# Performance work log

Hardware: AMD Instinct MI355X
Metric: run time of the kernel (lower is better)

Reference implementation:

```python
import jax, jax.numpy as jnp
import numpy as np

NUM_LEVELS = 8
CODEBOOK_SIZE = 1024
D_MODEL = 512


def setup_inputs() -> dict:
    key = jax.random.key(0)
    kx, kc = jax.random.split(key)
    x = jax.random.normal(kx, (8, 4096, D_MODEL), dtype=jnp.float32)
    # stacked embedding tables, one per RVQ level: [L, K, D]
    codebooks = jax.random.normal(kc, (NUM_LEVELS, CODEBOOK_SIZE, D_MODEL), dtype=jnp.float32)
    return {"x": x, "codebooks": codebooks}


def reference(x, codebooks):
    """Residual VQ: per level, nearest-codebook lookup on the residual.

    x: [B, N, D], codebooks: [L, K, D].
    Returns (quantized [B, N, D] with straight-through estimator, indices [B, N, L]).
    """
    residual = x
    q_sum = jnp.zeros_like(x)
    all_indices = []
    for l in range(codebooks.shape[0]):
        cb = codebooks[l]  # [K, D]
        # squared Euclidean distance; argmin matches torch.cdist argmin
        r2 = jnp.sum(residual * residual, axis=-1, keepdims=True)      # [B, N, 1]
        c2 = jnp.sum(cb * cb, axis=-1)                                  # [K]
        cross = jnp.einsum("bnd,kd->bnk", residual, cb)                # [B, N, K]
        dist2 = r2 - 2.0 * cross + c2                                   # [B, N, K]
        idx = jnp.argmin(dist2, axis=-1)                                # [B, N]
        all_indices.append(idx)
        q = cb[idx]                                                     # gather: [B, N, D]
        q_sum = q_sum + q
        residual = residual - q
    # straight-through: forward value is q_sum, gradient flows to x only
    quantized = x + jax.lax.stop_gradient(q_sum - x)
    return quantized, jnp.stack(all_indices, axis=-1)
```

## Files before the change

kernel.cpp:

```cpp
#include <hip/hip_runtime.h>
#include <stdint.h>

#define NLV 8
#define KCB 1024
#define DM  512
#define NTOK (8*4096)

typedef _Float16 f16;
typedef f16  f16x4 __attribute__((ext_vector_type(4)));
typedef f16  f16x8 __attribute__((ext_vector_type(8)));
typedef float f32x4 __attribute__((ext_vector_type(4)));

#define SPLIT_SCALE 2048.0f
#define INV_SPLIT   (1.0f/2048.0f)

typedef __attribute__((address_space(1))) const unsigned int* as1p;
typedef __attribute__((address_space(3))) unsigned int*       as3p;
__device__ __forceinline__ void gll16(const void* g, void* l) {
    __builtin_amdgcn_global_load_lds((as1p)g, (as3p)l, 16, 0, 0);
}

__global__ void c2_kernel(const float* __restrict__ cbs, float* __restrict__ c2) {
    int row  = blockIdx.x;
    int lane = threadIdx.x;
    const float4* p4 = (const float4*)(cbs + (size_t)row * DM);
    float4 a = p4[lane];
    float4 b = p4[lane + 64];
    float s = a.x*a.x + a.y*a.y + a.z*a.z + a.w*a.w
            + b.x*b.x + b.y*b.y + b.z*b.z + b.w*b.w;
    #pragma unroll
    for (int off = 32; off > 0; off >>= 1) s += __shfl_down(s, off, 64);
    if (lane == 0) c2[row] = s;
}

__global__ void split_kernel(const float* __restrict__ src,
                             f16* __restrict__ hi, f16* __restrict__ lo) {
    size_t i = (size_t)blockIdx.x * 256 + threadIdx.x;
    float4 v = ((const float4*)src)[i];
    f16x4 h, l;
    h.x = (f16)v.x; l.x = (f16)((v.x - (float)h.x) * SPLIT_SCALE);
    h.y = (f16)v.y; l.y = (f16)((v.y - (float)h.y) * SPLIT_SCALE);
    h.z = (f16)v.z; l.z = (f16)((v.z - (float)h.z) * SPLIT_SCALE);
    h.w = (f16)v.w; l.w = (f16)((v.w - (float)h.w) * SPLIT_SCALE);
    ((f16x4*)hi)[i] = h;
    ((f16x4*)lo)[i] = l;
}

#define MB   128
#define NCH  256
#define KS   32
#define NTHR 512
#define BUFB 49152

__global__ __launch_bounds__(NTHR, 2)
void rvq_mfma(const float* __restrict__ xin, float* __restrict__ qout,
              const float* __restrict__ cbs,
              const f16* __restrict__ Bhi, const f16* __restrict__ Blo,
              f16* __restrict__ Ahi, f16* __restrict__ Alo,
              const float* __restrict__ c2g, float* __restrict__ idxout,
              int lvl, int is_last)
{
    __shared__ char smem[2 * BUFB];
    const int tid  = threadIdx.x;
    const int lane = tid & 63;
    const int wid  = tid >> 6;
    const int wm   = wid >> 2;
    const int wn   = wid & 3;
    const int tx   = lane & 15;
    const int q    = lane >> 4;
    const size_t tok0 = (size_t)blockIdx.x * MB;

    const f16*   Bh_l = Bhi + (size_t)lvl * KCB * DM;
    const f16*   Bl_l = Blo + (size_t)lvl * KCB * DM;
    const float* c2l  = c2g + lvl * KCB;
    const float* cbl  = cbs + (size_t)lvl * KCB * DM;

    const int stg  = (tid & 3) ^ ((tid >> 3) & 3);
    const int srow = tid >> 2;
    const int rsw  = q ^ ((tx >> 1) & 3);

    auto stage = [&](char* bb, int cb0, int k0) {
        const int ko = k0 + stg * 8;
        const size_t arow = (tok0 + srow) * (size_t)DM + ko;
        gll16(&Ahi[arow], bb +     0 + wid * 1024);
        gll16(&Alo[arow], bb +  8192 + wid * 1024);
        const size_t br0 = (size_t)(cb0 + srow)       * DM + ko;
        const size_t br1 = (size_t)(cb0 + 128 + srow) * DM + ko;
        gll16(&Bh_l[br0], bb + 16384        + wid * 1024);
        gll16(&Bh_l[br1], bb + 16384 + 8192 + wid * 1024);
        gll16(&Bl_l[br0], bb + 32768        + wid * 1024);
        gll16(&Bl_l[br1], bb + 32768 + 8192 + wid * 1024);
    };

    float bestv[16];
    int   besti[16];
    #pragma unroll
    for (int t = 0; t < 16; ++t) { bestv[t] = 3.4e38f; besti[t] = 0; }

    stage(smem, 0, 0);

    for (int ch = 0; ch < KCB / NCH; ++ch) {
        const int cb0 = ch * NCH;
        f32x4 ahh[4][4], axx[4][4];
        #pragma unroll
        for (int i = 0; i < 4; ++i)
            #pragma unroll
            for (int j = 0; j < 4; ++j) { ahh[i][j] = (f32x4)0.0f; axx[i][j] = (f32x4)0.0f; }

        for (int kk = 0; kk < DM / KS; ++kk) {
            char* bb  = smem + (kk & 1) * BUFB;
            char* bbn = smem + ((kk & 1) ^ 1) * BUFB;
            __syncthreads();
            if (kk < DM / KS - 1)      stage(bbn, cb0, (kk + 1) * KS);
            else if (ch < KCB/NCH - 1) stage(bbn, cb0 + NCH, 0);

            const f16* sAh = (const f16*)(bb);
            const f16* sAl = (const f16*)(bb + 8192);
            const f16* sBh = (const f16*)(bb + 16384);
            const f16* sBl = (const f16*)(bb + 32768);

            f16x8 ah[4], al[4];
            #pragma unroll
            for (int i = 0; i < 4; ++i) {
                int off = (wm * 64 + i * 16 + tx) * 32 + rsw * 8;
                ah[i] = *(const f16x8*)&sAh[off];
                al[i] = *(const f16x8*)&sAl[off];
            }
            #pragma unroll
            for (int j = 0; j < 4; ++j) {
                int boff = (wn * 64 + j * 16 + tx) * 32 + rsw * 8;
                f16x8 bh = *(const f16x8*)&sBh[boff];
                f16x8 bl = *(const f16x8*)&sBl[boff];
                #pragma unroll
                for (int i = 0; i < 4; ++i) {
                    ahh[i][j] = __builtin_amdgcn_mfma_f32_16x16x32_f16(ah[i], bh, ahh[i][j], 0, 0, 0);
                    axx[i][j] = __builtin_amdgcn_mfma_f32_16x16x32_f16(ah[i], bl, axx[i][j], 0, 0, 0);
                    axx[i][j] = __builtin_amdgcn_mfma_f32_16x16x32_f16(al[i], bh, axx[i][j], 0, 0, 0);
                }
            }
        }

        #pragma unroll
        for (int j = 0; j < 4; ++j) {
            int n = cb0 + wn * 64 + j * 16 + tx;
            float c2v = c2l[n];
            #pragma unroll
            for (int i = 0; i < 4; ++i)
                #pragma unroll
                for (int r = 0; r < 4; ++r) {
                    float dot = ahh[i][j][r] + axx[i][j][r] * INV_SPLIT;
                    float s = fmaf(-2.f, dot, c2v);
                    int t = i * 4 + r;
                    if (s < bestv[t]) { bestv[t] = s; besti[t] = n; }
                }
        }
    }

    #pragma unroll
    for (int t = 0; t < 16; ++t) {
        float v = bestv[t]; int bi = besti[t];
        #pragma unroll
        for (int off = 1; off < 16; off <<= 1) {
            float ov = __shfl_xor(v, off, 64);
            int   oi = __shfl_xor(bi, off, 64);
            if (ov < v || (ov == v && oi < bi)) { v = ov; bi = oi; }
        }
        bestv[t] = v; besti[t] = bi;
    }

    float* redV = (float*)smem;
    int*   redI = (int*)(smem + 2048);
    int*   kbst = (int*)(smem + 4096);
    __syncthreads();
    if (tx == 0) {
        #pragma unroll
        for (int i = 0; i < 4; ++i)
            #pragma unroll
            for (int r = 0; r < 4; ++r) {
                int m = i * 16 + q * 4 + r;
                redV[(wm * 4 + wn) * 64 + m] = bestv[i * 4 + r];
                redI[(wm * 4 + wn) * 64 + m] = besti[i * 4 + r];
            }
    }
    __syncthreads();
    if (tid < MB) {
        int mwm = tid >> 6, m = tid & 63;
        float bv = redV[(mwm * 4) * 64 + m];
        int   bi = redI[(mwm * 4) * 64 + m];
        #pragma unroll
        for (int w = 1; w < 4; ++w) {
            float v  = redV[(mwm * 4 + w) * 64 + m];
            int   ii = redI[(mwm * 4 + w) * 64 + m];
            if (v < bv || (v == bv && ii < bi)) { bv = v; bi = ii; }
        }
        kbst[tid] = bi;
        idxout[(tok0 + tid) * NLV + lvl] = (float)bi;
    }
    __syncthreads();

    for (int it = 0; it < 16; ++it) {
        int e  = it * NTHR + tid;
        int t  = e >> 6, d8 = e & 63;
        size_t go = (tok0 + t) * (size_t)DM + d8 * 8;
        f16x8 h8 = *(const f16x8*)&Ahi[go];
        f16x8 l8 = *(const f16x8*)&Alo[go];
        const float* cp = &cbl[(size_t)kbst[t] * DM + d8 * 8];
        float4 c0 = *(const float4*)cp;
        float4 c1 = *(const float4*)(cp + 4);
        float r[8];
        r[0] = (float)h8[0] + (float)l8[0] * INV_SPLIT - c0.x;
        r[1] = (float)h8[1] + (float)l8[1] * INV_SPLIT - c0.y;
        r[2] = (float)h8[2] + (float)l8[2] * INV_SPLIT - c0.z;
        r[3] = (float)h8[3] + (float)l8[3] * INV_SPLIT - c0.w;
        r[4] = (float)h8[4] + (float)l8[4] * INV_SPLIT - c1.x;
        r[5] = (float)h8[5] + (float)l8[5] * INV_SPLIT - c1.y;
        r[6] = (float)h8[6] + (float)l8[6] * INV_SPLIT - c1.z;
        r[7] = (float)h8[7] + (float)l8[7] * INV_SPLIT - c1.w;
        if (is_last) {
            float4 x0 = *(const float4*)&xin[go];
            float4 x1 = *(const float4*)&xin[go + 4];
            float4 q0 = make_float4(x0.x - r[0], x0.y - r[1], x0.z - r[2], x0.w - r[3]);
            float4 q1 = make_float4(x1.x - r[4], x1.y - r[5], x1.z - r[6], x1.w - r[7]);
            *(float4*)&qout[go]     = q0;
            *(float4*)&qout[go + 4] = q1;
        } else {
            f16x8 h, l;
            #pragma unroll
            for (int k = 0; k < 8; ++k) {
                h[k] = (f16)r[k];
                l[k] = (f16)((r[k] - (float)h[k]) * SPLIT_SCALE);
            }
            *(f16x8*)&Ahi[go] = h;
            *(f16x8*)&Alo[go] = l;
        }
    }
}

extern "C" void kernel_launch(void* const* d_in, const int* in_sizes, int n_in,
                              void* d_out, int out_size, void* d_ws, size_t ws_size,
                              hipStream_t stream) {
    const float* x   = (const float*)d_in[0];
    const float* cbs = (const float*)d_in[1];
    float* qout   = (float*)d_out;
    float* idxout = qout + (size_t)NTOK * DM;

    const size_t B_ELE = (size_t)NLV * KCB * DM;
    const size_t A_ELE = (size_t)NTOK * DM;

    f16* Bhi = (f16*)d_ws;
    f16* Blo = Bhi + B_ELE;
    f16* Ahi = Blo + B_ELE;
    f16* Alo = Ahi + A_ELE;
    float* c2 = (float*)(Alo + A_ELE);

    split_kernel<<<(int)(B_ELE / 4 / 256), 256, 0, stream>>>(cbs, Bhi, Blo);
    split_kernel<<<(int)(A_ELE / 4 / 256), 256, 0, stream>>>(x, Ahi, Alo);
    c2_kernel<<<NLV * KCB, 64, 0, stream>>>(cbs, c2);

    const int nblocks = NTOK / MB;
    for (int l = 0; l < NLV; ++l) {
        rvq_mfma<<<nblocks, NTHR, 0, stream>>>(x, qout, cbs,
                                               Bhi, Blo, Ahi, Alo, c2, idxout,
                                               l, (l == NLV - 1) ? 1 : 0);
    }
}
```

Baseline: 1.152 ms.

## Shrink token tile, load A from registers, fold split correction into one accumulator

```diff
diff --git a/kernel.cpp b/kernel.cpp
--- a/kernel.cpp
+++ b/kernel.cpp
@@ -5,14 +5,12 @@
 #define KCB 1024
 #define DM  512
 #define NTOK (8*4096)
+#define BETA 0.00390625f
 
 typedef _Float16 f16;
 typedef f16  f16x4 __attribute__((ext_vector_type(4)));
 typedef f16  f16x8 __attribute__((ext_vector_type(8)));
 typedef float f32x4 __attribute__((ext_vector_type(4)));
-
-#define SPLIT_SCALE 2048.0f
-#define INV_SPLIT   (1.0f/2048.0f)
 
 typedef __attribute__((address_space(1))) const unsigned int* as1p;
 typedef __attribute__((address_space(3))) unsigned int*       as3p;
@@ -28,9 +26,14 @@
     float4 b = p4[lane + 64];
     float s = a.x*a.x + a.y*a.y + a.z*a.z + a.w*a.w
             + b.x*b.x + b.y*b.y + b.z*b.z + b.w*b.w;
-    #pragma unroll
-    for (int off = 32; off > 0; off >>= 1) s += __shfl_down(s, off, 64);
-    if (lane == 0) c2[row] = s;
+    float t = (float)(f16)a.x + (float)(f16)a.y + (float)(f16)a.z + (float)(f16)a.w
+            + (float)(f16)b.x + (float)(f16)b.y + (float)(f16)b.z + (float)(f16)b.w;
+    #pragma unroll
+    for (int off = 32; off > 0; off >>= 1) {
+        s += __shfl_down(s, off, 64);
+        t += __shfl_down(t, off, 64);
+    }
+    if (lane == 0) c2[row] = s + 2.0f * BETA * t;
 }
 
 __global__ void split_kernel(const float* __restrict__ src,
@@ -38,21 +41,20 @@
     size_t i = (size_t)blockIdx.x * 256 + threadIdx.x;
     float4 v = ((const float4*)src)[i];
     f16x4 h, l;
-    h.x = (f16)v.x; l.x = (f16)((v.x - (float)h.x) * SPLIT_SCALE);
-    h.y = (f16)v.y; l.y = (f16)((v.y - (float)h.y) * SPLIT_SCALE);
-    h.z = (f16)v.z; l.z = (f16)((v.z - (float)h.z) * SPLIT_SCALE);
-    h.w = (f16)v.w; l.w = (f16)((v.w - (float)h.w) * SPLIT_SCALE);
+    h.x = (f16)v.x; l.x = (f16)((v.x - (float)h.x) + BETA);
+    h.y = (f16)v.y; l.y = (f16)((v.y - (float)h.y) + BETA);
+    h.z = (f16)v.z; l.z = (f16)((v.z - (float)h.z) + BETA);
+    h.w = (f16)v.w; l.w = (f16)((v.w - (float)h.w) + BETA);
     ((f16x4*)hi)[i] = h;
     ((f16x4*)lo)[i] = l;
 }
 
-#define MB   128
+#define MBT  64
 #define NCH  256
 #define KS   32
 #define NTHR 512
-#define BUFB 49152
-
-__global__ __launch_bounds__(NTHR, 2)
+
+__global__ __launch_bounds__(NTHR, 4)
 void rvq_mfma(const float* __restrict__ xin, float* __restrict__ qout,
               const float* __restrict__ cbs,
               const f16* __restrict__ Bhi, const f16* __restrict__ Blo,
@@ -60,7 +62,7 @@
               const float* __restrict__ c2g, float* __restrict__ idxout,
               int lvl, int is_last)
 {
-    __shared__ char smem[2 * BUFB];
+    __shared__ char smem[65536];
     const int tid  = threadIdx.x;
     const int lane = tid & 63;
     const int wid  = tid >> 6;
@@ -68,75 +70,87 @@
     const int wn   = wid & 3;
     const int tx   = lane & 15;
     const int q    = lane >> 4;
-    const size_t tok0 = (size_t)blockIdx.x * MB;
+    const size_t tok0 = (size_t)blockIdx.x * MBT;
 
     const f16*   Bh_l = Bhi + (size_t)lvl * KCB * DM;
     const f16*   Bl_l = Blo + (size_t)lvl * KCB * DM;
     const float* c2l  = c2g + lvl * KCB;
     const float* cbl  = cbs + (size_t)lvl * KCB * DM;
 
-    const int stg  = (tid & 3) ^ ((tid >> 3) & 3);
     const int srow = tid >> 2;
-    const int rsw  = q ^ ((tx >> 1) & 3);
-
-    auto stage = [&](char* bb, int cb0, int k0) {
-        const int ko = k0 + stg * 8;
-        const size_t arow = (tok0 + srow) * (size_t)DM + ko;
-        gll16(&Ahi[arow], bb +     0 + wid * 1024);
-        gll16(&Alo[arow], bb +  8192 + wid * 1024);
-        const size_t br0 = (size_t)(cb0 + srow)       * DM + ko;
-        const size_t br1 = (size_t)(cb0 + 128 + srow) * DM + ko;
-        gll16(&Bh_l[br0], bb + 16384        + wid * 1024);
-        gll16(&Bh_l[br1], bb + 16384 + 8192 + wid * 1024);
-        gll16(&Bl_l[br0], bb + 32768        + wid * 1024);
-        gll16(&Bl_l[br1], bb + 32768 + 8192 + wid * 1024);
+    const int sg   = (tid & 3) ^ ((srow >> 1) & 3);
+    auto stageB = [&](char* buf, int cb0, int k0) {
+        const int ko = k0 + sg * 8;
+        const size_t g0 = (size_t)(cb0 + srow) * DM + ko;
+        const size_t g1 = g0 + (size_t)128 * DM;
+        char* l0 = buf + wid * 1024;
+        gll16(&Bh_l[g0], l0);
+        gll16(&Bh_l[g1], l0 + 8192);
+        gll16(&Bl_l[g0], l0 + 16384);
+        gll16(&Bl_l[g1], l0 + 16384 + 8192);
     };
 
-    float bestv[16];
-    int   besti[16];
-    #pragma unroll
-    for (int t = 0; t < 16; ++t) { bestv[t] = 3.4e38f; besti[t] = 0; }
-
-    stage(smem, 0, 0);
+    int boff[4];
+    #pragma unroll
+    for (int j = 0; j < 4; ++j) {
+        int row = wn * 64 + j * 16 + tx;
+        boff[j] = row * 64 + (q ^ ((tx >> 1) & 3)) * 16;
+    }
+
+    const f16* aH = Ahi + (tok0 + wm * 32 + tx) * (size_t)DM + q * 8;
+    const f16* aL = Alo + (tok0 + wm * 32 + tx) * (size_t)DM + q * 8;
+
+    float bestv[8];
+    int   besti[8];
+    #pragma unroll
+    for (int t = 0; t < 8; ++t) { bestv[t] = 3.4e38f; besti[t] = 0; }
+
+    f16x8 Ah[2][2], Al[2][2];
+    #pragma unroll
+    for (int i = 0; i < 2; ++i) {
+        Ah[0][i] = *(const f16x8*)(aH + i * 16 * DM);
+        Al[0][i] = *(const f16x8*)(aL + i * 16 * DM);
+    }
+    stageB(smem, 0, 0);
 
     for (int ch = 0; ch < KCB / NCH; ++ch) {
         const int cb0 = ch * NCH;
-        f32x4 ahh[4][4], axx[4][4];
-        #pragma unroll
-        for (int i = 0; i < 4; ++i)
-            #pragma unroll
-            for (int j = 0; j < 4; ++j) { ahh[i][j] = (f32x4)0.0f; axx[i][j] = (f32x4)0.0f; }
-
-        for (int kk = 0; kk < DM / KS; ++kk) {
-            char* bb  = smem + (kk & 1) * BUFB;
-            char* bbn = smem + ((kk & 1) ^ 1) * BUFB;
-            __syncthreads();
-            if (kk < DM / KS - 1)      stage(bbn, cb0, (kk + 1) * KS);
-            else if (ch < KCB/NCH - 1) stage(bbn, cb0 + NCH, 0);
-
-            const f16* sAh = (const f16*)(bb);
-            const f16* sAl = (const f16*)(bb + 8192);
-            const f16* sBh = (const f16*)(bb + 16384);
-            const f16* sBl = (const f16*)(bb + 32768);
-
-            f16x8 ah[4], al[4];
-            #pragma unroll
-            for (int i = 0; i < 4; ++i) {
-                int off = (wm * 64 + i * 16 + tx) * 32 + rsw * 8;
-                ah[i] = *(const f16x8*)&sAh[off];
-                al[i] = *(const f16x8*)&sAl[off];
-            }
-            #pragma unroll
-            for (int j = 0; j < 4; ++j) {
-                int boff = (wn * 64 + j * 16 + tx) * 32 + rsw * 8;
-                f16x8 bh = *(const f16x8*)&sBh[boff];
-                f16x8 bl = *(const f16x8*)&sBl[boff];
-                #pragma unroll
-                for (int i = 0; i < 4; ++i) {
-                    ahh[i][j] = __builtin_amdgcn_mfma_f32_16x16x32_f16(ah[i], bh, ahh[i][j], 0, 0, 0);
-                    axx[i][j] = __builtin_amdgcn_mfma_f32_16x16x32_f16(ah[i], bl, axx[i][j], 0, 0, 0);
-                    axx[i][j] = __builtin_amdgcn_mfma_f32_16x16x32_f16(al[i], bh, axx[i][j], 0, 0, 0);
+        f32x4 acc[2][4];
+        #pragma unroll
+        for (int i = 0; i < 2; ++i)
+            #pragma unroll
+            for (int j = 0; j < 4; ++j) acc[i][j] = (f32x4)0.0f;
+
+        for (int kh = 0; kh < 8; ++kh) {
+            #pragma unroll
+            for (int u = 0; u < 2; ++u) {
+                const int gk = ch * 16 + kh * 2 + u;
+                char* bb = smem + u * 32768;
+                char* bn = smem + (u ^ 1) * 32768;
+                __syncthreads();
+                if (gk + 1 < 64)
+                    stageB(bn, ((gk + 1) >> 4) * NCH, ((gk + 1) & 15) * KS);
+
+                f16x8 bh[4], bl[4];
+                #pragma unroll
+                for (int j = 0; j < 4; ++j) {
+                    bh[j] = *(const f16x8*)(bb + boff[j]);
+                    bl[j] = *(const f16x8*)(bb + 16384 + boff[j]);
                 }
+                const int nk = ((gk + 1) & 15) * KS;
+                #pragma unroll
+                for (int i = 0; i < 2; ++i) {
+                    Ah[u ^ 1][i] = *(const f16x8*)(aH + i * 16 * DM + nk);
+                    Al[u ^ 1][i] = *(const f16x8*)(aL + i * 16 * DM + nk);
+                }
+                #pragma unroll
+                for (int j = 0; j < 4; ++j)
+                    #pragma unroll
+                    for (int i = 0; i < 2; ++i) {
+                        acc[i][j] = __builtin_amdgcn_mfma_f32_16x16x32_f16(Ah[u][i], bh[j], acc[i][j], 0, 0, 0);
+                        acc[i][j] = __builtin_amdgcn_mfma_f32_16x16x32_f16(Ah[u][i], bl[j], acc[i][j], 0, 0, 0);
+                        acc[i][j] = __builtin_amdgcn_mfma_f32_16x16x32_f16(Al[u][i], bh[j], acc[i][j], 0, 0, 0);
+                    }
             }
         }
 
@@ -145,11 +159,10 @@
             int n = cb0 + wn * 64 + j * 16 + tx;
             float c2v = c2l[n];
             #pragma unroll
-            for (int i = 0; i < 4; ++i)
+            for (int i = 0; i < 2; ++i)
                 #pragma unroll
                 for (int r = 0; r < 4; ++r) {
-                    float dot = ahh[i][j][r] + axx[i][j][r] * INV_SPLIT;
-                    float s = fmaf(-2.f, dot, c2v);
+                    float s = fmaf(-2.f, acc[i][j][r], c2v);
                     int t = i * 4 + r;
                     if (s < bestv[t]) { bestv[t] = s; besti[t] = n; }
                 }
@@ -157,7 +170,7 @@
     }
 
     #pragma unroll
-    for (int t = 0; t < 16; ++t) {
+    for (int t = 0; t < 8; ++t) {
         float v = bestv[t]; int bi = besti[t];
         #pragma unroll
         for (int off = 1; off < 16; off <<= 1) {
@@ -169,28 +182,28 @@
     }
 
     float* redV = (float*)smem;
-    int*   redI = (int*)(smem + 2048);
-    int*   kbst = (int*)(smem + 4096);
+    int*   redI = (int*)(smem + 1024);
+    int*   kbst = (int*)(smem + 2048);
     __syncthreads();
     if (tx == 0) {
         #pragma unroll
-        for (int i = 0; i < 4; ++i)
+        for (int i = 0; i < 2; ++i)
             #pragma unroll
             for (int r = 0; r < 4; ++r) {
                 int m = i * 16 + q * 4 + r;
-                redV[(wm * 4 + wn) * 64 + m] = bestv[i * 4 + r];
-                redI[(wm * 4 + wn) * 64 + m] = besti[i * 4 + r];
+                redV[(wm * 4 + wn) * 32 + m] = bestv[i * 4 + r];
+                redI[(wm * 4 + wn) * 32 + m] = besti[i * 4 + r];
             }
     }
     __syncthreads();
-    if (tid < MB) {
-        int mwm = tid >> 6, m = tid & 63;
-        float bv = redV[(mwm * 4) * 64 + m];
-        int   bi = redI[(mwm * 4) * 64 + m];
+    if (tid < MBT) {
+        int strip = tid >> 5, m = tid & 31;
+        float bv = redV[(strip * 4) * 32 + m];
+        int   bi = redI[(strip * 4) * 32 + m];
         #pragma unroll
         for (int w = 1; w < 4; ++w) {
-            float v  = redV[(mwm * 4 + w) * 64 + m];
-            int   ii = redI[(mwm * 4 + w) * 64 + m];
+            float v  = redV[(strip * 4 + w) * 32 + m];
+            int   ii = redI[(strip * 4 + w) * 32 + m];
             if (v < bv || (v == bv && ii < bi)) { bv = v; bi = ii; }
         }
         kbst[tid] = bi;
@@ -198,7 +211,7 @@
     }
     __syncthreads();
 
-    for (int it = 0; it < 16; ++it) {
+    for (int it = 0; it < 8; ++it) {
         int e  = it * NTHR + tid;
         int t  = e >> 6, d8 = e & 63;
         size_t go = (tok0 + t) * (size_t)DM + d8 * 8;
@@ -208,14 +221,14 @@
         float4 c0 = *(const float4*)cp;
         float4 c1 = *(const float4*)(cp + 4);
         float r[8];
-        r[0] = (float)h8[0] + (float)l8[0] * INV_SPLIT - c0.x;
-        r[1] = (float)h8[1] + (float)l8[1] * INV_SPLIT - c0.y;
-        r[2] = (float)h8[2] + (float)l8[2] * INV_SPLIT - c0.z;
-        r[3] = (float)h8[3] + (float)l8[3] * INV_SPLIT - c0.w;
-        r[4] = (float)h8[4] + (float)l8[4] * INV_SPLIT - c1.x;
-        r[5] = (float)h8[5] + (float)l8[5] * INV_SPLIT - c1.y;
-        r[6] = (float)h8[6] + (float)l8[6] * INV_SPLIT - c1.z;
-        r[7] = (float)h8[7] + (float)l8[7] * INV_SPLIT - c1.w;
+        r[0] = (float)h8[0] + ((float)l8[0] - BETA) - c0.x;
+        r[1] = (float)h8[1] + ((float)l8[1] - BETA) - c0.y;
+        r[2] = (float)h8[2] + ((float)l8[2] - BETA) - c0.z;
+        r[3] = (float)h8[3] + ((float)l8[3] - BETA) - c0.w;
+        r[4] = (float)h8[4] + ((float)l8[4] - BETA) - c1.x;
+        r[5] = (float)h8[5] + ((float)l8[5] - BETA) - c1.y;
+        r[6] = (float)h8[6] + ((float)l8[6] - BETA) - c1.z;
+        r[7] = (float)h8[7] + ((float)l8[7] - BETA) - c1.w;
         if (is_last) {
             float4 x0 = *(const float4*)&xin[go];
             float4 x1 = *(const float4*)&xin[go + 4];
@@ -228,7 +241,7 @@
             #pragma unroll
             for (int k = 0; k < 8; ++k) {
                 h[k] = (f16)r[k];
-                l[k] = (f16)((r[k] - (float)h[k]) * SPLIT_SCALE);
+                l[k] = (f16)((r[k] - (float)h[k]) + BETA);
             }
             *(f16x8*)&Ahi[go] = h;
             *(f16x8*)&Alo[go] = l;
@@ -257,7 +270,7 @@
     split_kernel<<<(int)(A_ELE / 4 / 256), 256, 0, stream>>>(x, Ahi, Alo);
     c2_kernel<<<NLV * KCB, 64, 0, stream>>>(cbs, c2);
 
-    const int nblocks = NTOK / MB;
+    const int nblocks = NTOK / MBT;
     for (int l = 0; l < NLV; ++l) {
         rvq_mfma<<<nblocks, NTHR, 0, stream>>>(x, qout, cbs,
                                                Bhi, Blo, Ahi, Alo, c2, idxout,
```

After: 1.618 ms. 40.5% more time.
